# Kernel optimization log

Hardware: AMD Instinct MI355X
Metric: run time of the kernel (lower is better)

## Reference

```python
import jax, jax.numpy as jnp
import numpy as np


def setup_inputs() -> dict:
    key = jax.random.key(0)
    k1, k2, k3 = jax.random.split(key, 3)
    I, H, W, C, N = 8, 240, 320, 128, 100000
    img_feats = jax.random.normal(k1, (I, H, W, C), dtype=jnp.float32)
    pcd_feats = jax.random.normal(k2, (N, C), dtype=jnp.float32)
    # pixel coords in [0, 360): values >= H (or >= W) are masked out, mimicking
    # points that project outside the image (compute_masks)
    pcd_pixels = jax.random.randint(k3, (I, N, 2), 0, 360, dtype=jnp.int32)
    return {"img_feats": img_feats, "pcd_feats": pcd_feats, "pcd_pixels": pcd_pixels}


def reference(img_feats, pcd_feats, pcd_pixels):
    # img_feats: [I, H, W, C], pcd_feats: [N, C], pcd_pixels: [I, N, 2] (h, w)
    I, H, W, C = img_feats.shape
    N = pcd_feats.shape[0]
    h = pcd_pixels[..., 0]
    w = pcd_pixels[..., 1]
    # compute_masks: in-bounds check
    mask = (h >= 0) & (h < H) & (w >= 0) & (w < W)            # [I, N] bool
    m = mask.astype(img_feats.dtype)                          # [I, N]
    hc = jnp.clip(h, 0, H - 1)
    wc = jnp.clip(w, 0, W - 1)
    flat_hw = hc * W + wc                                     # [I, N]

    # ---- collect_img_feats: gather image feats at pixels, mean over images per point
    gathered = jnp.take_along_axis(
        img_feats.reshape(I, H * W, C), flat_hw[..., None], axis=1
    )                                                         # [I, N, C]
    pcd_counts = m.sum(axis=0)                                # [N]
    pcd_from_img = (gathered * m[..., None]).sum(axis=0) / jnp.clip(
        pcd_counts, 1e-10
    )[:, None]                                                # [N, C]

    # ---- collect_pcd_feats: scatter point feats into image grid, mean per pixel
    flat_idx = (jnp.arange(I, dtype=flat_hw.dtype)[:, None] * (H * W) + flat_hw).reshape(-1)  # [I*N]
    src = (pcd_feats[None, :, :] * m[..., None]).reshape(-1, C)                               # [I*N, C]
    img_sum = jnp.zeros((I * H * W, C), img_feats.dtype).at[flat_idx].add(src)
    img_cnt = jnp.zeros((I * H * W,), img_feats.dtype).at[flat_idx].add(m.reshape(-1))
    img_from_pcd = (img_sum / jnp.clip(img_cnt, 1e-10)[:, None]).reshape(I, H, W, C)

    return pcd_from_img, img_from_pcd
```

## Files before the change

kernel.cpp:

```cpp
#include <hip/hip_runtime.h>

#define IMGS 8
#define HH 240
#define WW 320
#define CC 128
#define HW (HH * WW)
#define ELEMS (IMGS * HW)

#define CAP 16

typedef float f4 __attribute__((ext_vector_type(4)));

__global__ __launch_bounds__(256) void zero_counts_kernel(uint4* __restrict__ p)
{
    int t = blockIdx.x * 256 + threadIdx.x;
    if (t < ELEMS / 4) p[t] = make_uint4(0u, 0u, 0u, 0u);
}

__global__ __launch_bounds__(256) void prep_count_fill_kernel(
    const int* __restrict__ pix,
    unsigned*  __restrict__ counts,
    unsigned*  __restrict__ list,
    unsigned*  __restrict__ poff,
    int N)
{
    int n = blockIdx.x * 256 + threadIdx.x;
    if (n >= N) return;

    unsigned po[IMGS];
#pragma unroll
    for (int i = 0; i < IMGS; ++i) {
        int2 hw = *reinterpret_cast<const int2*>(pix + ((size_t)i * N + n) * 2);
        int h = hw.x, w = hw.y;
        bool ok = (h >= 0) & (h < HH) & (w >= 0) & (w < WW);
        int hc = min(max(h, 0), HH - 1);
        int wc = min(max(w, 0), WW - 1);
        unsigned off = (unsigned)(i * HW + hc * WW + wc);
        po[i] = off | (ok ? 0x80000000u : 0u);
        if (ok) {
            unsigned slot = atomicAdd(&counts[off], 1u);
            if (slot < CAP) list[(size_t)off * CAP + slot] = (unsigned)n;
        }
    }
    uint4* dst = reinterpret_cast<uint4*>(poff + (size_t)n * IMGS);
    dst[0] = make_uint4(po[0], po[1], po[2], po[3]);
    dst[1] = make_uint4(po[4], po[5], po[6], po[7]);
}

#define GB 12500
#define TOTAL 89600

__global__ __launch_bounds__(256) void mega_kernel(
    const f4*       __restrict__ img4,
    const unsigned* __restrict__ poff,
    const f4*       __restrict__ pcd4,
    const unsigned* __restrict__ counts,
    const unsigned* __restrict__ list,
    float*          __restrict__ out_pcd,
    float*          __restrict__ out_img,
    int N)
{
    int bid = blockIdx.x;
    if (bid % 7 == 0) {
        int gb = bid / 7;
        if (gb >= GB) return;
        int tid   = gb * 256 + threadIdx.x;
        int point = tid >> 5;
        int lane  = tid & 31;
        if (point >= N) return;

        const uint4* pp = reinterpret_cast<const uint4*>(poff + (size_t)point * IMGS);
        uint4 pa = pp[0], pb = pp[1];
        unsigned po[IMGS] = {pa.x, pa.y, pa.z, pa.w, pb.x, pb.y, pb.z, pb.w};

        f4    v[IMGS];
        float m[IMGS];
#pragma unroll
        for (int i = 0; i < IMGS; ++i) {
            unsigned off = po[i] & 0x7fffffffu;
            v[i] = img4[(size_t)off * 32u + (unsigned)lane];
            m[i] = (po[i] & 0x80000000u) ? 1.f : 0.f;
        }
        __builtin_amdgcn_sched_barrier(0);

        f4 acc = {0.f, 0.f, 0.f, 0.f};
        float cnt = 0.f;
#pragma unroll
        for (int i = 0; i < IMGS; ++i) {
            acc += v[i] * m[i];
            cnt += m[i];
        }
        float inv = 1.f / fmaxf(cnt, 1e-10f);
        acc *= inv;
        __builtin_nontemporal_store(
            acc, reinterpret_cast<f4*>(out_pcd + (size_t)point * CC) + lane);
    } else {
        int ob   = bid - bid / 7 - 1;
        int tid  = ob * 256 + threadIdx.x;
        int p    = tid >> 5;
        int lane = tid & 31;

        unsigned kc = counts[p];
        uint4 L = reinterpret_cast<const uint4*>(list + (size_t)p * CAP)[0];

        unsigned k = kc < CAP ? kc : CAP;
        f4 acc = {0.f, 0.f, 0.f, 0.f};
        if (k) {
            unsigned id[4] = {L.x, L.y, L.z, L.w};
            f4 v[4];
#pragma unroll
            for (int t = 0; t < 4; ++t) {
                unsigned idx = ((unsigned)t < k) ? id[t] : id[0];
                v[t] = pcd4[(size_t)idx * 32u + (unsigned)lane];
            }
#pragma unroll
            for (int t = 0; t < 4; ++t)
                acc += v[t] * (((unsigned)t < k) ? 1.f : 0.f);

            for (unsigned base = 4; base < k; base += 4) {
                uint4 L2 = reinterpret_cast<const uint4*>(list + (size_t)p * CAP)[base >> 2];
                unsigned id2[4] = {L2.x, L2.y, L2.z, L2.w};
                f4 v2[4];
#pragma unroll
                for (int t = 0; t < 4; ++t) {
                    unsigned idx = (base + t < k) ? id2[t] : id2[0];
                    v2[t] = pcd4[(size_t)idx * 32u + (unsigned)lane];
                }
#pragma unroll
                for (int t = 0; t < 4; ++t)
                    acc += v2[t] * ((base + t < k) ? 1.f : 0.f);
            }
        }
        float inv = 1.f / fmaxf((float)kc, 1e-10f);
        acc *= inv;
        __builtin_nontemporal_store(
            acc, reinterpret_cast<f4*>(out_img + (size_t)p * CC) + lane);
    }
}

__global__ __launch_bounds__(256) void gather_kernel(
    const float* __restrict__ img, const int* __restrict__ pix,
    float* __restrict__ out, int N)
{
    int tid   = blockIdx.x * blockDim.x + threadIdx.x;
    int point = tid >> 5;
    int lane  = tid & 31;
    if (point >= N) return;
    f4 acc = {0.f, 0.f, 0.f, 0.f};
    float cnt = 0.f;
#pragma unroll
    for (int i = 0; i < IMGS; ++i) {
        int2 hw = *reinterpret_cast<const int2*>(pix + ((size_t)i * N + point) * 2);
        int h = hw.x, w = hw.y;
        if (h >= 0 && h < HH && w >= 0 && w < WW) {
            acc += reinterpret_cast<const f4*>(
                img + ((size_t)i * HW + (size_t)h * WW + w) * CC)[lane];
            cnt += 1.f;
        }
    }
    float inv = 1.f / fmaxf(cnt, 1e-10f);
    acc *= inv;
    reinterpret_cast<f4*>(out + (size_t)point * CC)[lane] = acc;
}

__global__ __launch_bounds__(256) void scatter_kernel(
    const float* __restrict__ pcd, const int* __restrict__ pix,
    float* __restrict__ img_sum, float* __restrict__ cnt, int N)
{
    int n = blockIdx.x * 2 + (threadIdx.x >> 7);
    int c = threadIdx.x & 127;
    int i = blockIdx.y;
    if (n >= N) return;
    int2 hw = *reinterpret_cast<const int2*>(pix + ((size_t)i * N + n) * 2);
    int h = hw.x, w = hw.y;
    if (h >= 0 && h < HH && w >= 0 && w < WW) {
        size_t p = (size_t)i * HW + (size_t)h * WW + w;
        atomicAdd(&img_sum[p * CC + c], pcd[(size_t)n * CC + c]);
        if (c == 0) atomicAdd(&cnt[p], 1.f);
    }
}

__global__ __launch_bounds__(256) void normalize_kernel(
    float* __restrict__ img_sum, const float* __restrict__ cnt)
{
    int tid  = blockIdx.x * blockDim.x + threadIdx.x;
    int pixI = tid >> 5;
    int lane = tid & 31;
    if (pixI >= ELEMS) return;
    float inv = 1.f / fmaxf(cnt[pixI], 1e-10f);
    f4* p = reinterpret_cast<f4*>(img_sum + (size_t)pixI * CC) + lane;
    f4 v = *p;
    v *= inv;
    *p = v;
}

extern "C" void kernel_launch(void* const* d_in, const int* in_sizes, int n_in,
                              void* d_out, int out_size, void* d_ws, size_t ws_size,
                              hipStream_t stream)
{
    const float* img_feats  = (const float*)d_in[0];
    const float* pcd_feats  = (const float*)d_in[1];
    const int*   pcd_pixels = (const int*)d_in[2];

    const int N = in_sizes[1] / CC;

    float* out_pcd = (float*)d_out;
    float* out_img = out_pcd + (size_t)N * CC;

    size_t need = (size_t)ELEMS * 4
                + (size_t)ELEMS * CAP * 4
                + (size_t)N * IMGS * 4;

    if (ws_size >= need) {
        unsigned* counts = (unsigned*)d_ws;
        unsigned* list   = counts + ELEMS;
        unsigned* poff   = list + (size_t)ELEMS * CAP;

        zero_counts_kernel<<<(ELEMS / 4 + 255) / 256, 256, 0, stream>>>((uint4*)counts);

        prep_count_fill_kernel<<<(N + 255) / 256, 256, 0, stream>>>(
            pcd_pixels, counts, list, poff, N);

        mega_kernel<<<TOTAL, 256, 0, stream>>>(
            (const f4*)img_feats, poff, (const f4*)pcd_feats,
            counts, list, out_pcd, out_img, N);
    } else {
        {
            int blocks = (N * 32 + 255) / 256;
            gather_kernel<<<blocks, 256, 0, stream>>>(img_feats, pcd_pixels, out_pcd, N);
        }
        float* cnt = (float*)d_ws;
        hipMemsetAsync(out_img, 0, (size_t)ELEMS * CC * sizeof(float), stream);
        hipMemsetAsync(cnt,     0, (size_t)ELEMS * sizeof(float), stream);
        dim3 sgrid((N + 1) / 2, IMGS, 1);
        scatter_kernel<<<sgrid, 256, 0, stream>>>(pcd_feats, pcd_pixels, out_img, cnt, N);
        long long t = (long long)ELEMS * 32;
        int blocks  = (int)((t + 255) / 256);
        normalize_kernel<<<blocks, 256, 0, stream>>>(out_img, cnt);
    }
}
```

Before: 189.9 us.

## Process four pixels per warp group in scatter-mean branch, rebalance block interleave

The image-side branch of the fused kernel now has each 32-lane group handle four consecutive pixels. It loads their counts with one vector load and issues the first point-feature load for all four up front, so memory-level parallelism goes up and the block count drops. The block interleave changes from 1-of-7 to 2-of-5 gather blocks to match the new ratio, and the scheduling barrier in the gather branch is removed. The trade-off is more per-thread work and serial inner loops for pixels with many hits, which could lower occupancy or add latency.

After: 182.1 us (median of 2 runs). 4.1% less time.

```diff
diff --git a/kernel.cpp b/kernel.cpp
--- a/kernel.cpp
+++ b/kernel.cpp
@@ -48,7 +48,7 @@
 }
 
 #define GB 12500
-#define TOTAL 89600
+#define TOTAL 32000
 
 __global__ __launch_bounds__(256) void mega_kernel(
     const f4*       __restrict__ img4,
@@ -61,8 +61,9 @@
     int N)
 {
     int bid = blockIdx.x;
-    if (bid % 7 == 0) {
-        int gb = bid / 7;
+    int r5  = bid % 5;
+    if (r5 < 2) {
+        int gb = (bid / 5) * 2 + r5;
         if (gb >= GB) return;
         int tid   = gb * 256 + threadIdx.x;
         int point = tid >> 5;
@@ -79,9 +80,8 @@
         for (int i = 0; i < IMGS; ++i) {
             unsigned off = po[i] & 0x7fffffffu;
             v[i] = img4[(size_t)off * 32u + (unsigned)lane];
-            m[i] = (po[i] & 0x80000000u) ? 1.f : 0.f;
-        }
-        __builtin_amdgcn_sched_barrier(0);
+            m[i] = (po[i] >> 31) ? 1.f : 0.f;
+        }
 
         f4 acc = {0.f, 0.f, 0.f, 0.f};
         float cnt = 0.f;
@@ -95,46 +95,44 @@
         __builtin_nontemporal_store(
             acc, reinterpret_cast<f4*>(out_pcd + (size_t)point * CC) + lane);
     } else {
-        int ob   = bid - bid / 7 - 1;
-        int tid  = ob * 256 + threadIdx.x;
-        int p    = tid >> 5;
-        int lane = tid & 31;
-
-        unsigned kc = counts[p];
-        uint4 L = reinterpret_cast<const uint4*>(list + (size_t)p * CAP)[0];
-
-        unsigned k = kc < CAP ? kc : CAP;
-        f4 acc = {0.f, 0.f, 0.f, 0.f};
-        if (k) {
-            unsigned id[4] = {L.x, L.y, L.z, L.w};
-            f4 v[4];
-#pragma unroll
-            for (int t = 0; t < 4; ++t) {
-                unsigned idx = ((unsigned)t < k) ? id[t] : id[0];
-                v[t] = pcd4[(size_t)idx * 32u + (unsigned)lane];
+        int ob    = (bid / 5) * 3 + r5 - 2;
+        int grp   = threadIdx.x >> 5;
+        int lane  = threadIdx.x & 31;
+        int pbase = ob * 32 + grp * 4;
+
+        uint4 KC = *reinterpret_cast<const uint4*>(counts + pbase);
+        unsigned kcs[4] = {KC.x, KC.y, KC.z, KC.w};
+        uint4 L[4];
+#pragma unroll
+        for (int j = 0; j < 4; ++j)
+            L[j] = reinterpret_cast<const uint4*>(list + (size_t)(pbase + j) * CAP)[0];
+
+        f4 r[4];
+#pragma unroll
+        for (int j = 0; j < 4; ++j) {
+            unsigned idx = kcs[j] ? L[j].x : 0u;
+            r[j] = pcd4[(size_t)idx * 32u + (unsigned)lane];
+        }
+
+#pragma unroll
+        for (int j = 0; j < 4; ++j) {
+            f4 acc = r[j] * (kcs[j] ? 1.f : 0.f);
+            unsigned k = kcs[j] < CAP ? kcs[j] : CAP;
+            if (k > 1) {
+                unsigned ids[3] = {L[j].y, L[j].z, L[j].w};
+#pragma unroll
+                for (unsigned t = 1; t < 4; ++t)
+                    if (t < k)
+                        acc += pcd4[(size_t)ids[t - 1] * 32u + (unsigned)lane];
+                for (unsigned t = 4; t < k; ++t)
+                    acc += pcd4[(size_t)list[(size_t)(pbase + j) * CAP + t] * 32u
+                                + (unsigned)lane];
             }
-#pragma unroll
-            for (int t = 0; t < 4; ++t)
-                acc += v[t] * (((unsigned)t < k) ? 1.f : 0.f);
-
-            for (unsigned base = 4; base < k; base += 4) {
-                uint4 L2 = reinterpret_cast<const uint4*>(list + (size_t)p * CAP)[base >> 2];
-                unsigned id2[4] = {L2.x, L2.y, L2.z, L2.w};
-                f4 v2[4];
-#pragma unroll
-                for (int t = 0; t < 4; ++t) {
-                    unsigned idx = (base + t < k) ? id2[t] : id2[0];
-                    v2[t] = pcd4[(size_t)idx * 32u + (unsigned)lane];
-                }
-#pragma unroll
-                for (int t = 0; t < 4; ++t)
-                    acc += v2[t] * ((base + t < k) ? 1.f : 0.f);
-            }
-        }
-        float inv = 1.f / fmaxf((float)kc, 1e-10f);
-        acc *= inv;
-        __builtin_nontemporal_store(
-            acc, reinterpret_cast<f4*>(out_img + (size_t)p * CC) + lane);
+            float inv = 1.f / fmaxf((float)kcs[j], 1e-10f);
+            acc *= inv;
+            __builtin_nontemporal_store(
+                acc, reinterpret_cast<f4*>(out_img + (size_t)(pbase + j) * CC) + lane);
+        }
     }
 }
 
```
